# Kernel tuning notes

Hardware: AMD Instinct MI355X
Metric: run time of the kernel (lower is better)

The kernel has to match this reference:

```python
import jax, jax.numpy as jnp
import numpy as np

D_MODEL = 1024
N_HEADS = 16
D_K = D_MODEL // N_HEADS
D_FF = 4096
B, S = 2, 2048
LN_EPS = 1e-5
NEG_INF = -1e30  # finite stand-in for -inf; first (all-masked) row is overwritten by zeros anyway


def layer_norm(x, g, b):
    mu = jnp.mean(x, axis=-1, keepdims=True)
    var = jnp.mean(jnp.square(x - mu), axis=-1, keepdims=True)
    return (x - mu) * jax.lax.rsqrt(var + LN_EPS) * g + b


def setup_inputs() -> dict:
    key = jax.random.key(0)
    ks = jax.random.split(key, 16)
    sd = 0.02
    inp = {
        "query": jax.random.normal(ks[0], (B, S, D_MODEL), jnp.float32),
        "key": jax.random.normal(ks[1], (B, S, D_MODEL), jnp.float32),
        "values": jax.random.normal(ks[2], (B, S, D_MODEL), jnp.float32),
        "Wq": jax.random.normal(ks[3], (D_MODEL, D_MODEL), jnp.float32) * sd,
        "bq": jnp.zeros((D_MODEL,), jnp.float32),
        "Wk": jax.random.normal(ks[4], (D_MODEL, D_MODEL), jnp.float32) * sd,
        "bk": jnp.zeros((D_MODEL,), jnp.float32),
        "Wv": jax.random.normal(ks[5], (D_MODEL, D_MODEL), jnp.float32) * sd,
        "bv": jnp.zeros((D_MODEL,), jnp.float32),
        "Wo": jax.random.normal(ks[6], (D_MODEL, D_MODEL), jnp.float32) * sd,
        "bo": jnp.zeros((D_MODEL,), jnp.float32),
        "ln1_g": jnp.ones((D_MODEL,), jnp.float32),
        "ln1_b": jnp.zeros((D_MODEL,), jnp.float32),
        "W1": jax.random.normal(ks[7], (D_MODEL, D_FF), jnp.float32) * sd,
        "b1": jnp.zeros((D_FF,), jnp.float32),
        "W2": jax.random.normal(ks[8], (D_FF, D_MODEL), jnp.float32) * sd,
        "b2": jnp.zeros((D_MODEL,), jnp.float32),
        "ln2_g": jnp.ones((D_MODEL,), jnp.float32),
        "ln2_b": jnp.zeros((D_MODEL,), jnp.float32),
        "mask": 0,
    }
    return inp


def reference(query, key, values, Wq, bq, Wk, bk, Wv, bv, Wo, bo,
              ln1_g, ln1_b, W1, b1, W2, b2, ln2_g, ln2_b, mask):
    b, s, d = query.shape
    # projections -> [B, H, S, d_k]
    q = (query @ Wq + bq).reshape(b, s, N_HEADS, D_K).transpose(0, 2, 1, 3)
    k = (key @ Wk + bk).reshape(b, s, N_HEADS, D_K).transpose(0, 2, 1, 3)
    v = (values @ Wv + bv).reshape(b, s, N_HEADS, D_K).transpose(0, 2, 1, 3)
    # scores [B, H, S, S]
    scores = jnp.einsum("bhqd,bhkd->bhqk", q, k) / jnp.sqrt(jnp.float32(D_K))
    # torch: triu(ones, k=mask)==0 -> allowed iff j < i + mask
    i = jnp.arange(s)[:, None]
    j = jnp.arange(s)[None, :]
    allowed = j < (i + mask)
    scores = jnp.where(allowed, scores, NEG_INF)
    attn = jax.nn.softmax(scores, axis=-1)
    if mask == 0:
        # zero-pad trick: first query row (fully masked) is replaced by zeros
        attn = attn.at[:, :, 0, :].set(0.0)
    ctx = jnp.einsum("bhqk,bhkd->bhqd", attn, v)
    ctx = ctx.transpose(0, 2, 1, 3).reshape(b, s, d)
    attn_out = ctx @ Wo + bo
    x = layer_norm(query + attn_out, ln1_g, ln1_b)
    ffn = jax.nn.relu(x @ W1 + b1) @ W2 + b2
    out = layer_norm(x + ffn, ln2_g, ln2_b)
    return out
```

## Files before the change

### kernel.cpp

```cpp
#include <hip/hip_runtime.h>


typedef __attribute__((ext_vector_type(8))) __bf16 bf16x8;
typedef __attribute__((ext_vector_type(4))) float f32x4;
typedef __attribute__((ext_vector_type(8))) short s16x8;

struct alignas(8)  S4 { short x, y, z, w; };
struct alignas(16) F4 { float x, y, z, w; };

static __device__ __forceinline__ short f2bf(float f) {
  unsigned u = __float_as_uint(f);
  u += 0x7fff + ((u >> 16) & 1);
  return (short)(u >> 16);
}

static __device__ __forceinline__ short f2bf_fast(float f) {
  union { __bf16 h; short s; } u;
  u.h = (__bf16)f;
  return u.s;
}

#if __has_builtin(__builtin_amdgcn_exp2f)
#define EXP2F(x) __builtin_amdgcn_exp2f(x)
#else
#define EXP2F(x) exp2f(x)
#endif
#define SM_SCALE 0.18033688011112042f

static __device__ __forceinline__ void store_out(float* p, float v) { *p = v; }
static __device__ __forceinline__ void store_out(short* p, float v) { *p = f2bf(v); }

#define GLL16(g, l)                                                         \
  __builtin_amdgcn_global_load_lds(                                         \
      (__attribute__((address_space(1))) void*)(g),                         \
      (__attribute__((address_space(3))) void*)(l), 16, 0, 0)

__global__ __launch_bounds__(256) void cvt_bf16_kernel(
    const float* __restrict__ i0, const float* __restrict__ i1,
    const float* __restrict__ i2, short* __restrict__ o0,
    short* __restrict__ o1, short* __restrict__ o2) {
  int z = blockIdx.y;
  const float* in = z == 0 ? i0 : (z == 1 ? i1 : i2);
  short* out = z == 0 ? o0 : (z == 1 ? o1 : o2);
  int i = (blockIdx.x * 256 + threadIdx.x) * 4;
  F4 v = *(const F4*)(in + i);
  S4 o = { f2bf(v.x), f2bf(v.y), f2bf(v.z), f2bf(v.w) };
  *(S4*)(out + i) = o;
}

__global__ __launch_bounds__(256) void transpose_cvt_kernel(
    const float* __restrict__ Wq, const float* __restrict__ Wk,
    const float* __restrict__ Wv, const float* __restrict__ Wo,
    const float* __restrict__ W1, const float* __restrict__ W2,
    short* __restrict__ Wqt, short* __restrict__ Wkt,
    short* __restrict__ Wvt, short* __restrict__ Wot,
    short* __restrict__ W1t, short* __restrict__ W2t) {
  __shared__ float tile[64][65];
  int bid = blockIdx.x;
  const float* W; short* Wt; int K, N, kx, ny;
  if (bid < 1024) {
    int w = bid >> 8, t = bid & 255;
    W = w == 0 ? Wq : (w == 1 ? Wk : (w == 2 ? Wv : Wo));
    Wt = w == 0 ? Wqt : (w == 1 ? Wkt : (w == 2 ? Wvt : Wot));
    K = 1024; N = 1024; kx = t & 15; ny = t >> 4;
  } else if (bid < 2048) {
    int t = bid - 1024;
    W = W1; Wt = W1t; K = 1024; N = 4096; kx = t & 15; ny = t >> 4;
  } else {
    int t = bid - 2048;
    W = W2; Wt = W2t; K = 4096; N = 1024; kx = t & 63; ny = t >> 6;
  }
  int k0 = kx * 64, n0 = ny * 64;
  int tid = threadIdx.x;
  int rr = tid >> 4, cc = (tid & 15) * 4;
#pragma unroll
  for (int p = 0; p < 4; ++p) {
    int row = p * 16 + rr;
    F4 v = *(const F4*)&W[(long)(k0 + row) * N + n0 + cc];
    tile[row][cc] = v.x; tile[row][cc + 1] = v.y;
    tile[row][cc + 2] = v.z; tile[row][cc + 3] = v.w;
  }
  __syncthreads();
#pragma unroll
  for (int p = 0; p < 4; ++p) {
    int rn = p * 16 + rr;
    S4 o = { f2bf(tile[cc + 0][rn]), f2bf(tile[cc + 1][rn]),
             f2bf(tile[cc + 2][rn]), f2bf(tile[cc + 3][rn]) };
    *(S4*)&Wt[(long)(n0 + rn) * K + k0 + cc] = o;
  }
}

template <int NF, int OUT_MODE, bool RELU, typename OT>
__device__ __forceinline__ void gemm256_core(
    const short* __restrict__ A, const short* __restrict__ Bt,
    const float* __restrict__ bias, OT* __restrict__ out,
    int N, int K, int kBeg, int kEnd, int m0, int n0) {
  constexpr int BN = NF * 64;
  constexpr int LB = BN / 64;
  __shared__ __align__(16) short sA[2][256 * 64];
  __shared__ __align__(16) short sB[2][BN * 64];
  int tid = threadIdx.x;
  int lane = tid & 63, wave = tid >> 6;
  int col = lane & 15, quad = lane >> 4;
  int wm = (wave >> 2) * 128;
  int wn = (wave & 3) * (NF * 16);

  f32x4 acc[8][NF] = {};

  const int NT = (kEnd - kBeg) >> 6;
  const int t0 = kBeg >> 6;

  auto stageA = [&](int buf, int kt) {
#pragma unroll
    for (int j = 0; j < 4; ++j) {
      int idx = j * 512 + tid;
      int row = idx >> 3, cp = idx & 7;
      int c = cp ^ (row & 7);
      GLL16(A + (long)(m0 + row) * K + kt * 64 + c * 8,
            &sA[buf][(j * 512 + (wave << 6)) * 8]);
    }
  };
  auto stageB = [&](int buf, int kt) {
#pragma unroll
    for (int j = 0; j < LB; ++j) {
      int idx = j * 512 + tid;
      int row = idx >> 3, cp = idx & 7;
      int c = cp ^ (row & 7);
      GLL16(Bt + (long)(n0 + row) * K + kt * 64 + c * 8,
            &sB[buf][(j * 512 + (wave << 6)) * 8]);
    }
  };

  stageA(0, t0);     stageB(0, t0);
  stageA(1, t0 + 1); stageB(1, t0 + 1);
  if constexpr (NF == 4) asm volatile("s_waitcnt vmcnt(8)" ::: "memory");
  else                   asm volatile("s_waitcnt vmcnt(6)" ::: "memory");
  __builtin_amdgcn_sched_barrier(0);
  __builtin_amdgcn_s_barrier();

  for (int t = 0; t < NT; ++t) {
    int cur = t & 1;
    bool pf = (t + 2 < NT);
    bf16x8 bf[NF][2], af[2][2];

#pragma unroll
    for (int n = 0; n < NF; ++n) {
      int rb = wn + n * 16 + col;
#pragma unroll
      for (int kk = 0; kk < 2; ++kk) {
        int ca = kk * 4 + quad;
        bf[n][kk] = *(const bf16x8*)&sB[cur][rb * 64 + ((ca ^ (rb & 7)) << 3)];
      }
    }
#pragma unroll
    for (int i = 0; i < 2; ++i) {
      int ra = wm + i * 16 + col;
#pragma unroll
      for (int kk = 0; kk < 2; ++kk) {
        int ca = kk * 4 + quad;
        af[i][kk] = *(const bf16x8*)&sA[cur][ra * 64 + ((ca ^ (ra & 7)) << 3)];
      }
    }
    asm volatile("s_waitcnt lgkmcnt(0)" ::: "memory");
    __builtin_amdgcn_sched_barrier(0);
    __builtin_amdgcn_s_setprio(1);
#pragma unroll
    for (int i = 0; i < 2; ++i)
#pragma unroll
      for (int n = 0; n < NF; ++n)
#pragma unroll
        for (int kk = 0; kk < 2; ++kk)
          acc[i][n] = __builtin_amdgcn_mfma_f32_16x16x32_bf16(
              af[i][kk], bf[n][kk], acc[i][n], 0, 0, 0);
    __builtin_amdgcn_s_setprio(0);
    __builtin_amdgcn_s_barrier();
    __builtin_amdgcn_sched_barrier(0);

    if (pf) stageB(cur, t0 + t + 2);
#pragma unroll
    for (int i = 0; i < 2; ++i) {
      int ra = wm + (2 + i) * 16 + col;
#pragma unroll
      for (int kk = 0; kk < 2; ++kk) {
        int ca = kk * 4 + quad;
        af[i][kk] = *(const bf16x8*)&sA[cur][ra * 64 + ((ca ^ (ra & 7)) << 3)];
      }
    }
    __builtin_amdgcn_s_setprio(1);
#pragma unroll
    for (int i = 0; i < 2; ++i)
#pragma unroll
      for (int n = 0; n < NF; ++n)
#pragma unroll
        for (int kk = 0; kk < 2; ++kk)
          acc[2 + i][n] = __builtin_amdgcn_mfma_f32_16x16x32_bf16(
              af[i][kk], bf[n][kk], acc[2 + i][n], 0, 0, 0);
    __builtin_amdgcn_s_setprio(0);
    __builtin_amdgcn_s_barrier();

#pragma unroll
    for (int i = 0; i < 2; ++i) {
      int ra = wm + (4 + i) * 16 + col;
#pragma unroll
      for (int kk = 0; kk < 2; ++kk) {
        int ca = kk * 4 + quad;
        af[i][kk] = *(const bf16x8*)&sA[cur][ra * 64 + ((ca ^ (ra & 7)) << 3)];
      }
    }
    __builtin_amdgcn_s_setprio(1);
#pragma unroll
    for (int i = 0; i < 2; ++i)
#pragma unroll
      for (int n = 0; n < NF; ++n)
#pragma unroll
        for (int kk = 0; kk < 2; ++kk)
          acc[4 + i][n] = __builtin_amdgcn_mfma_f32_16x16x32_bf16(
              af[i][kk], bf[n][kk], acc[4 + i][n], 0, 0, 0);
    __builtin_amdgcn_s_setprio(0);
    __builtin_amdgcn_s_barrier();

#pragma unroll
    for (int i = 0; i < 2; ++i) {
      int ra = wm + (6 + i) * 16 + col;
#pragma unroll
      for (int kk = 0; kk < 2; ++kk) {
        int ca = kk * 4 + quad;
        af[i][kk] = *(const bf16x8*)&sA[cur][ra * 64 + ((ca ^ (ra & 7)) << 3)];
      }
    }
    asm volatile("s_waitcnt lgkmcnt(0)" ::: "memory");
    __builtin_amdgcn_sched_barrier(0);
    __builtin_amdgcn_s_barrier();
    __builtin_amdgcn_sched_barrier(0);
    if (pf) stageA(cur, t0 + t + 2);
    __builtin_amdgcn_s_setprio(1);
#pragma unroll
    for (int i = 0; i < 2; ++i)
#pragma unroll
      for (int n = 0; n < NF; ++n)
#pragma unroll
        for (int kk = 0; kk < 2; ++kk)
          acc[6 + i][n] = __builtin_amdgcn_mfma_f32_16x16x32_bf16(
              af[i][kk], bf[n][kk], acc[6 + i][n], 0, 0, 0);
    __builtin_amdgcn_s_setprio(0);
    if (pf) {
      if constexpr (NF == 4) asm volatile("s_waitcnt vmcnt(8)" ::: "memory");
      else                   asm volatile("s_waitcnt vmcnt(6)" ::: "memory");
    } else {
      asm volatile("s_waitcnt vmcnt(0)" ::: "memory");
    }
    __builtin_amdgcn_sched_barrier(0);
    __builtin_amdgcn_s_barrier();
  }

#pragma unroll
  for (int m = 0; m < 8; ++m) {
#pragma unroll
    for (int n = 0; n < NF; ++n) {
      int Cc = n0 + wn + n * 16 + col;
      float bv = bias ? bias[Cc] : 0.f;
#pragma unroll
      for (int r = 0; r < 4; ++r) {
        int R = m0 + wm + m * 16 + quad * 4 + r;
        float v = acc[m][n][r] + bv;
        if (RELU) v = v > 0.f ? v : 0.f;
        if (OUT_MODE == 0) {
          store_out(&out[(long)R * N + Cc], v);
        } else {
          int bb = R >> 11, s = R & 2047, h = Cc >> 6, d = Cc & 63;
          store_out(&out[((long)((bb * 16 + h) * 2048 + s) << 6) + d], v);
        }
      }
    }
  }
}

__device__ __forceinline__ void gsp128_core(
    const short* __restrict__ A, const short* __restrict__ Bt,
    const float* __restrict__ bias, float* __restrict__ out,
    int N, int K, int kBeg, int kEnd, int m0, int n0) {
  __shared__ __align__(16) short sA[2][256 * 64];
  __shared__ __align__(16) short sB[2][128 * 64];
  int tid = threadIdx.x;
  int lane = tid & 63, wave = tid >> 6;
  int col = lane & 15, quad = lane >> 4;
  int wm = (wave >> 1) * 64;
  int wn = (wave & 1) * 64;

  f32x4 acc[4][4] = {};
  const int NT = (kEnd - kBeg) >> 6;
  const int t0 = kBeg >> 6;

  auto stageA = [&](int buf, int kt) {
#pragma unroll
    for (int j = 0; j < 4; ++j) {
      int idx = j * 512 + tid;
      int row = idx >> 3, cp = idx & 7;
      int c = cp ^ (row & 7);
      GLL16(A + (long)(m0 + row) * K + kt * 64 + c * 8,
            &sA[buf][(j * 512 + (wave << 6)) * 8]);
    }
  };
  auto stageB = [&](int buf, int kt) {
#pragma unroll
    for (int j = 0; j < 2; ++j) {
      int idx = j * 512 + tid;
      int row = idx >> 3, cp = idx & 7;
      int c = cp ^ (row & 7);
      GLL16(Bt + (long)(n0 + row) * K + kt * 64 + c * 8,
            &sB[buf][(j * 512 + (wave << 6)) * 8]);
    }
  };

  stageA(0, t0);     stageB(0, t0);
  stageA(1, t0 + 1); stageB(1, t0 + 1);
  asm volatile("s_waitcnt vmcnt(6)" ::: "memory");
  __builtin_amdgcn_s_barrier();

  for (int t = 0; t < NT; ++t) {
    int cur = t & 1;
    bool pf = (t + 2 < NT);
    bf16x8 bf[4][2], af[4][2];

#pragma unroll
    for (int n = 0; n < 4; ++n) {
      int rb = wn + n * 16 + col;
#pragma unroll
      for (int kk = 0; kk < 2; ++kk) {
        int ca = kk * 4 + quad;
        bf[n][kk] = *(const bf16x8*)&sB[cur][rb * 64 + ((ca ^ (rb & 7)) << 3)];
      }
    }
#pragma unroll
    for (int m = 0; m < 4; ++m) {
      int ra = wm + m * 16 + col;
#pragma unroll
      for (int kk = 0; kk < 2; ++kk) {
        int ca = kk * 4 + quad;
        af[m][kk] = *(const bf16x8*)&sA[cur][ra * 64 + ((ca ^ (ra & 7)) << 3)];
      }
    }
    asm volatile("s_waitcnt lgkmcnt(0)" ::: "memory");
    __builtin_amdgcn_s_barrier();
    __builtin_amdgcn_sched_barrier(0);
    if (pf) { stageA(cur, t0 + t + 2); stageB(cur, t0 + t + 2); }
    __builtin_amdgcn_s_setprio(1);
#pragma unroll
    for (int m = 0; m < 4; ++m)
#pragma unroll
      for (int n = 0; n < 4; ++n)
#pragma unroll
        for (int kk = 0; kk < 2; ++kk)
          acc[m][n] = __builtin_amdgcn_mfma_f32_16x16x32_bf16(
              af[m][kk], bf[n][kk], acc[m][n], 0, 0, 0);
    __builtin_amdgcn_s_setprio(0);
    if (pf) asm volatile("s_waitcnt vmcnt(6)" ::: "memory");
    else    asm volatile("s_waitcnt vmcnt(0)" ::: "memory");
    __builtin_amdgcn_s_barrier();
  }

#pragma unroll
  for (int m = 0; m < 4; ++m) {
#pragma unroll
    for (int n = 0; n < 4; ++n) {
      int Cc = n0 + wn + n * 16 + col;
      float bv = bias ? bias[Cc] : 0.f;
#pragma unroll
      for (int r = 0; r < 4; ++r) {
        int R = m0 + wm + m * 16 + quad * 4 + r;
        out[(long)R * N + Cc] = acc[m][n][r] + bv;
      }
    }
  }
}

__global__ __launch_bounds__(512) void g256_ffn1(
    const short* __restrict__ A, const short* __restrict__ Bt,
    const float* __restrict__ bias, short* __restrict__ out) {
  gemm256_core<4, 0, true, short>(A, Bt, bias, out, 4096, 1024, 0, 1024,
                                  blockIdx.x * 256, blockIdx.y * 256);
}

__global__ __launch_bounds__(512) void g256_qkv(
    const short* __restrict__ Aq, const short* __restrict__ Ak,
    const short* __restrict__ Av, const short* __restrict__ Btq,
    const short* __restrict__ Btk, const short* __restrict__ Btv,
    const float* __restrict__ bq, const float* __restrict__ bk,
    const float* __restrict__ bv, short* __restrict__ Qp,
    short* __restrict__ Kp, short* __restrict__ Vp) {
  int z = blockIdx.z;
  const short* A = z == 0 ? Aq : (z == 1 ? Ak : Av);
  const short* Bt = z == 0 ? Btq : (z == 1 ? Btk : Btv);
  const float* bias = z == 0 ? bq : (z == 1 ? bk : bv);
  short* out = z == 0 ? Qp : (z == 1 ? Kp : Vp);
  gemm256_core<4, 1, false, short>(A, Bt, bias, out, 1024, 1024, 0, 1024,
                                   blockIdx.x * 256, blockIdx.y * 256);
}

__global__ __launch_bounds__(512) void gsp_wo(
    const short* __restrict__ A, const short* __restrict__ Bt,
    const float* __restrict__ bias, float* __restrict__ p0,
    float* __restrict__ p1) {
  int z = blockIdx.z;
  float* out = z == 0 ? p0 : p1;
  const float* b = z == 0 ? bias : nullptr;
  gsp128_core(A, Bt, b, out, 1024, 1024, z * 512, z * 512 + 512,
              blockIdx.x * 256, blockIdx.y * 128);
}

__global__ __launch_bounds__(512) void gsp_ffn2(
    const short* __restrict__ A, const short* __restrict__ Bt,
    const float* __restrict__ bias, float* __restrict__ p0,
    float* __restrict__ p1) {
  int z = blockIdx.z;
  float* out = z == 0 ? p0 : p1;
  const float* b = z == 0 ? bias : nullptr;
  gsp128_core(A, Bt, b, out, 1024, 4096, z * 2048, z * 2048 + 2048,
              blockIdx.x * 256, blockIdx.y * 128);
}

__global__ __launch_bounds__(256) void attn_kernel(
    const short* __restrict__ Q, const short* __restrict__ K,
    const short* __restrict__ V, const int* __restrict__ maskp,
    short* __restrict__ ctx) {
  __shared__ __align__(16) short sK[2][64 * 64];
  __shared__ __align__(16) int   sVt[2][64 * 32];
  __shared__ __align__(16) short sP[4 * 32 * 64];
  __shared__ float sLred[64];
  int tid = threadIdx.x, wave = tid >> 6;
  int lane = tid & 63;
  int col = lane & 15, quad = lane >> 4;
  int wlow = wave >> 1, g = wave & 1;
  int bh = blockIdx.x, pair = blockIdx.y;
  int maskv = maskp[0];
  const long base = (long)bh * (2048 * 64);
  int b = bh >> 4, h = bh & 15;

  int kp = tid & 31, dg = tid >> 5, d0v = dg * 8;

  for (int pass = 0; pass < 2; ++pass) {
    int qt = pass ? (31 - pair) : pair;
    int iq0 = qt * 64 + wlow * 32;

    long jmax = (long)qt * 64 + 63 + maskv - 1;
    int tot = (jmax < 0) ? 0 : (int)(jmax >> 6) + 1;
    if (tot > 32) tot = 32;

    bf16x8 aQ[2][2];
#pragma unroll
    for (int mt = 0; mt < 2; ++mt)
#pragma unroll
      for (int kk = 0; kk < 2; ++kk)
        aQ[mt][kk] = *(const bf16x8*)&Q[base +
            (long)(iq0 + mt * 16 + col) * 64 + kk * 32 + quad * 8];

    f32x4 o[2][4] = {};
    float lsum[2][4] = {};

    if (tot > 0) {
#pragma unroll
      for (int j = 0; j < 2; ++j) {
        int idx = j * 256 + tid;
        int row = idx >> 3, cp = idx & 7;
        int c = cp ^ (row & 7);
        GLL16(K + base + (long)row * 64 + c * 8,
              &sK[0][(j * 256 + (wave << 6)) * 8]);
      }
      {
        s16x8 u0 = *(const s16x8*)&V[base + (long)(2 * kp) * 64 + d0v];
        s16x8 u1 = *(const s16x8*)&V[base + (long)(2 * kp + 1) * 64 + d0v];
#pragma unroll
        for (int j = 0; j < 8; ++j) {
          int d = d0v + j;
          int w = ((int)(unsigned short)u1[j] << 16) | (unsigned short)u0[j];
          sVt[0][d * 32 + ((((kp >> 2) ^ (d & 7)) << 2) | (kp & 3))] = w;
        }
      }
    }
    __syncthreads();

    for (int kt = 0; kt < tot; ++kt) {
      int cur = kt & 1, nxt = cur ^ 1;
      bool pf = (kt + 1 < tot);

      s16x8 u0, u1;
      if (pf) {
#pragma unroll
        for (int j = 0; j < 2; ++j) {
          int idx = j * 256 + tid;
          int row = idx >> 3, cp = idx & 7;
          int c = cp ^ (row & 7);
          GLL16(K + base + (long)((kt + 1) * 64 + row) * 64 + c * 8,
                &sK[nxt][(j * 256 + (wave << 6)) * 8]);
        }
        u0 = *(const s16x8*)&V[base + (long)((kt + 1) * 64 + 2 * kp) * 64 + d0v];
        u1 = *(const s16x8*)&V[base + (long)((kt + 1) * 64 + 2 * kp + 1) * 64 + d0v];
      }

      f32x4 sc[2][2] = {};
      __builtin_amdgcn_s_setprio(1);
#pragma unroll
      for (int kk = 0; kk < 2; ++kk) {
        int ca = kk * 4 + quad;
#pragma unroll
        for (int nt = 0; nt < 2; ++nt) {
          int rk = (2 * g + nt) * 16 + col;
          bf16x8 bK = *(const bf16x8*)&sK[cur][rk * 64 + ((ca ^ (rk & 7)) << 3)];
#pragma unroll
          for (int mt = 0; mt < 2; ++mt)
            sc[mt][nt] = __builtin_amdgcn_mfma_f32_16x16x32_bf16(
                aQ[mt][kk], bK, sc[mt][nt], 0, 0, 0);
        }
      }
      __builtin_amdgcn_s_setprio(0);

      bool interior = (kt * 64 + g * 32 + 31) < (iq0 + maskv);
      if (interior) {
#pragma unroll
        for (int mt = 0; mt < 2; ++mt)
#pragma unroll
          for (int r = 0; r < 4; ++r) {
            int qr = mt * 16 + quad * 4 + r;
#pragma unroll
            for (int nt = 0; nt < 2; ++nt) {
              float p = EXP2F(sc[mt][nt][r] * SM_SCALE);
              lsum[mt][r] += p;
              int k8 = 4 * g + nt * 2 + (col >> 3);
              sP[wave * 2048 + qr * 64 + (((k8 ^ (qr & 7)) << 3) | (col & 7))] =
                  f2bf_fast(p);
            }
          }
      } else {
#pragma unroll
        for (int mt = 0; mt < 2; ++mt)
#pragma unroll
          for (int r = 0; r < 4; ++r) {
            int i = iq0 + mt * 16 + quad * 4 + r;
            int qr = mt * 16 + quad * 4 + r;
#pragma unroll
            for (int nt = 0; nt < 2; ++nt) {
              int j = kt * 64 + (2 * g + nt) * 16 + col;
              float p = (j < i + maskv) ? EXP2F(sc[mt][nt][r] * SM_SCALE) : 0.f;
              lsum[mt][r] += p;
              int k8 = 4 * g + nt * 2 + (col >> 3);
              sP[wave * 2048 + qr * 64 + (((k8 ^ (qr & 7)) << 3) | (col & 7))] =
                  f2bf_fast(p);
            }
          }
      }

      {
        int ca = 4 * g + quad;
        bf16x8 bV[4];
#pragma unroll
        for (int dt = 0; dt < 4; ++dt) {
          int d = dt * 16 + col;
          bV[dt] = *(const bf16x8*)((const short*)sVt[cur] + d * 64 +
                                    ((ca ^ (d & 7)) << 3));
        }
        __builtin_amdgcn_s_setprio(1);
#pragma unroll
        for (int mt = 0; mt < 2; ++mt) {
          int rp = mt * 16 + col;
          bf16x8 aP = *(const bf16x8*)&sP[wave * 2048 + rp * 64 +
                                          ((ca ^ (rp & 7)) << 3)];
#pragma unroll
          for (int dt = 0; dt < 4; ++dt)
            o[mt][dt] = __builtin_amdgcn_mfma_f32_16x16x32_bf16(
                aP, bV[dt], o[mt][dt], 0, 0, 0);
        }
        __builtin_amdgcn_s_setprio(0);
      }

      if (pf) {
#pragma unroll
        for (int j = 0; j < 8; ++j) {
          int d = d0v + j;
          int w = ((int)(unsigned short)u1[j] << 16) | (unsigned short)u0[j];
          sVt[nxt][d * 32 + ((((kp >> 2) ^ (d & 7)) << 2) | (kp & 3))] = w;
        }
      }
      __syncthreads();
    }

#pragma unroll
    for (int mt = 0; mt < 2; ++mt)
#pragma unroll
      for (int r = 0; r < 4; ++r)
#pragma unroll
        for (int off = 1; off < 16; off <<= 1)
          lsum[mt][r] += __shfl_xor(lsum[mt][r], off);

    f32x4* odv = (f32x4*)sP;
    int slot = wlow * 64 + lane;
    if (g == 1) {
#pragma unroll
      for (int mt = 0; mt < 2; ++mt)
#pragma unroll
        for (int dt = 0; dt < 4; ++dt)
          odv[(mt * 4 + dt) * 128 + slot] = o[mt][dt];
      if (col == 0) {
#pragma unroll
        for (int mt = 0; mt < 2; ++mt)
#pragma unroll
          for (int r = 0; r < 4; ++r)
            sLred[wlow * 32 + mt * 16 + quad * 4 + r] = lsum[mt][r];
      }
    }
    __syncthreads();
    if (g == 0) {
#pragma unroll
      for (int mt = 0; mt < 2; ++mt)
#pragma unroll
        for (int dt = 0; dt < 4; ++dt)
          o[mt][dt] += odv[(mt * 4 + dt) * 128 + slot];
#pragma unroll
      for (int mt = 0; mt < 2; ++mt)
#pragma unroll
        for (int r = 0; r < 4; ++r) {
          float ls = lsum[mt][r] + sLred[wlow * 32 + mt * 16 + quad * 4 + r];
          int i = iq0 + mt * 16 + quad * 4 + r;
          float inv = (ls > 0.f) ? 1.f / ls : 0.f;
          if (maskv == 0 && i == 0) inv = 0.f;
#pragma unroll
          for (int dt = 0; dt < 4; ++dt)
            ctx[(long)(b * 2048 + i) * 1024 + h * 64 + dt * 16 + col] =
                f2bf(o[mt][dt][r] * inv);
        }
    }
    __syncthreads();
  }
}

__global__ __launch_bounds__(256) void ln_comb_kernel(
    const float* __restrict__ p0, const float* __restrict__ p1,
    const float* __restrict__ res, const float* __restrict__ g,
    const float* __restrict__ b, float* __restrict__ outf,
    short* __restrict__ outb) {
  int r = blockIdx.x, tid = threadIdx.x;
  int lane = tid & 63, wave = tid >> 6;
  long off0 = (long)r * 1024;
  F4 a = ((const F4*)(p0 + off0))[tid];
  F4 c = ((const F4*)(p1 + off0))[tid];
  F4 d = ((const F4*)(res + off0))[tid];
  F4 v = { a.x + c.x + d.x, a.y + c.y + d.y, a.z + c.z + d.z, a.w + c.w + d.w };
  float s = v.x + v.y + v.z + v.w;
  float sq = v.x * v.x + v.y * v.y + v.z * v.z + v.w * v.w;
#pragma unroll
  for (int off = 1; off < 64; off <<= 1) {
    s += __shfl_xor(s, off);
    sq += __shfl_xor(sq, off);
  }
  __shared__ float rs[4], rq[4];
  if (lane == 0) { rs[wave] = s; rq[wave] = sq; }
  __syncthreads();
  s = rs[0] + rs[1] + rs[2] + rs[3];
  sq = rq[0] + rq[1] + rq[2] + rq[3];
  float mu = s * (1.0f / 1024.0f);
  float var = sq * (1.0f / 1024.0f) - mu * mu;
  float rstd = rsqrtf(var + 1e-5f);
  F4 gv = ((const F4*)g)[tid], bv = ((const F4*)b)[tid];
  F4 o;
  o.x = (v.x - mu) * rstd * gv.x + bv.x;
  o.y = (v.y - mu) * rstd * gv.y + bv.y;
  o.z = (v.z - mu) * rstd * gv.z + bv.z;
  o.w = (v.w - mu) * rstd * gv.w + bv.w;
  ((F4*)(outf + off0))[tid] = o;
  if (outb) {
    S4 ob = { f2bf(o.x), f2bf(o.y), f2bf(o.z), f2bf(o.w) };
    ((S4*)(outb + off0))[tid] = ob;
  }
}

extern "C" void kernel_launch(void* const* d_in, const int* in_sizes, int n_in,
                              void* d_out, int out_size, void* d_ws, size_t ws_size,
                              hipStream_t stream) {
  const float* query  = (const float*)d_in[0];
  const float* keyi   = (const float*)d_in[1];
  const float* values = (const float*)d_in[2];
  const float* Wq = (const float*)d_in[3];
  const float* bq = (const float*)d_in[4];
  const float* Wk = (const float*)d_in[5];
  const float* bk = (const float*)d_in[6];
  const float* Wv = (const float*)d_in[7];
  const float* bv = (const float*)d_in[8];
  const float* Wo = (const float*)d_in[9];
  const float* bo = (const float*)d_in[10];
  const float* ln1_g = (const float*)d_in[11];
  const float* ln1_b = (const float*)d_in[12];
  const float* W1 = (const float*)d_in[13];
  const float* b1 = (const float*)d_in[14];
  const float* W2 = (const float*)d_in[15];
  const float* b2 = (const float*)d_in[16];
  const float* ln2_g = (const float*)d_in[17];
  const float* ln2_b = (const float*)d_in[18];
  const int*   maskp = (const int*)d_in[19];
  float* out = (float*)d_out;

  char* ws = (char*)d_ws;
  const size_t MB = 1u << 20;
  short* q_bf = (short*)(ws + 0);
  short* k_bf = (short*)(ws + 8 * MB);
  short* v_bf = (short*)(ws + 16 * MB);
  short* ctx  = (short*)(ws + 24 * MB);
  short* Qp   = (short*)(ws + 32 * MB);
  short* Kp   = (short*)(ws + 40 * MB);
  short* Vp   = (short*)(ws + 48 * MB);
  short* Wqt  = (short*)(ws + 56 * MB);
  short* Wkt  = (short*)(ws + 58 * MB);
  short* Wvt  = (short*)(ws + 60 * MB);
  short* Wot  = (short*)(ws + 62 * MB);
  short* W1t  = (short*)(ws + 64 * MB);
  short* W2t  = (short*)(ws + 72 * MB);
  short* hbuf = (short*)(ws + 80 * MB);
  float* pWo0 = (float*)(ws + 0);
  float* pWo1 = (float*)(ws + 32 * MB);
  float* x_f32 = (float*)(ws + 16 * MB);
  short* x_bf  = (short*)(ws + 48 * MB);
  float* pF0 = (float*)(ws + 0);
  float* pF1 = (float*)(ws + 32 * MB);

  cvt_bf16_kernel<<<dim3(4096, 3), 256, 0, stream>>>(query, keyi, values,
                                                     q_bf, k_bf, v_bf);
  transpose_cvt_kernel<<<3072, 256, 0, stream>>>(Wq, Wk, Wv, Wo, W1, W2,
                                                 Wqt, Wkt, Wvt, Wot, W1t, W2t);
  g256_qkv<<<dim3(16, 4, 3), 512, 0, stream>>>(q_bf, k_bf, v_bf,
                                               Wqt, Wkt, Wvt,
                                               bq, bk, bv, Qp, Kp, Vp);
  attn_kernel<<<dim3(32, 16), 256, 0, stream>>>(Qp, Kp, Vp, maskp, ctx);
  gsp_wo<<<dim3(16, 8, 2), 512, 0, stream>>>(ctx, Wot, bo, pWo0, pWo1);
  ln_comb_kernel<<<4096, 256, 0, stream>>>(pWo0, pWo1, query, ln1_g, ln1_b,
                                           x_f32, x_bf);
  g256_ffn1<<<dim3(16, 16), 512, 0, stream>>>(x_bf, W1t, b1, hbuf);
  gsp_ffn2<<<dim3(16, 8, 2), 512, 0, stream>>>(hbuf, W2t, b2, pF0, pF1);
  ln_comb_kernel<<<4096, 256, 0, stream>>>(pF0, pF1, x_f32, ln2_g, ln2_b,
                                           out, nullptr);

  (void)in_sizes; (void)n_in; (void)out_size; (void)ws_size;
}
```

Before: 371.1 us.

## Collapse 256x256 GEMM main loop into single load-all/compute-all phase per k-tile

Replaces the four-phase interleaved k-loop (A fragments loaded in pairs, with MFMA groups, barriers and staggered A/B prefetches between them) with a simpler schedule. Each k-tile now loads all A and B fragments from LDS, issues one barrier, prefetches both A and B for tile t+2, then runs all 64 MFMAs. This cuts barriers per iteration from four to two and removes the sched_barrier fences. In exchange it needs more registers for the 16 A fragments, and it gives up overlap of LDS reads with MFMA work, which may reduce occupancy or lengthen the issue latency.

```diff
diff --git a/kernel.cpp b/kernel.cpp
--- a/kernel.cpp
+++ b/kernel.cpp
@@ -90,23 +90,20 @@
   }
 }
 
-template <int NF, int OUT_MODE, bool RELU, typename OT>
-__device__ __forceinline__ void gemm256_core(
+template <int OUT_MODE, bool RELU, typename OT>
+__device__ __forceinline__ void gemm256c_core(
     const short* __restrict__ A, const short* __restrict__ Bt,
     const float* __restrict__ bias, OT* __restrict__ out,
     int N, int K, int kBeg, int kEnd, int m0, int n0) {
-  constexpr int BN = NF * 64;
-  constexpr int LB = BN / 64;
   __shared__ __align__(16) short sA[2][256 * 64];
-  __shared__ __align__(16) short sB[2][BN * 64];
+  __shared__ __align__(16) short sB[2][256 * 64];
   int tid = threadIdx.x;
   int lane = tid & 63, wave = tid >> 6;
   int col = lane & 15, quad = lane >> 4;
   int wm = (wave >> 2) * 128;
-  int wn = (wave & 3) * (NF * 16);
-
-  f32x4 acc[8][NF] = {};
-
+  int wn = (wave & 3) * 64;
+
+  f32x4 acc[8][4] = {};
   const int NT = (kEnd - kBeg) >> 6;
   const int t0 = kBeg >> 6;
 
@@ -122,7 +119,7 @@
   };
   auto stageB = [&](int buf, int kt) {
 #pragma unroll
-    for (int j = 0; j < LB; ++j) {
+    for (int j = 0; j < 4; ++j) {
       int idx = j * 512 + tid;
       int row = idx >> 3, cp = idx & 7;
       int c = cp ^ (row & 7);
@@ -133,18 +130,16 @@
 
   stageA(0, t0);     stageB(0, t0);
   stageA(1, t0 + 1); stageB(1, t0 + 1);
-  if constexpr (NF == 4) asm volatile("s_waitcnt vmcnt(8)" ::: "memory");
-  else                   asm volatile("s_waitcnt vmcnt(6)" ::: "memory");
-  __builtin_amdgcn_sched_barrier(0);
+  asm volatile("s_waitcnt vmcnt(8)" ::: "memory");
   __builtin_amdgcn_s_barrier();
 
   for (int t = 0; t < NT; ++t) {
     int cur = t & 1;
     bool pf = (t + 2 < NT);
-    bf16x8 bf[NF][2], af[2][2];
-
-#pragma unroll
-    for (int n = 0; n < NF; ++n) {
+    bf16x8 bf[4][2], af[8][2];
+
+#pragma unroll
+    for (int n = 0; n < 4; ++n) {
       int rb = wn + n * 16 + col;
 #pragma unroll
       for (int kk = 0; kk < 2; ++kk) {
@@ -153,110 +148,37 @@
       }
     }
 #pragma unroll
-    for (int i = 0; i < 2; ++i) {
-      int ra = wm + i * 16 + col;
+    for (int m = 0; m < 8; ++m) {
+      int ra = wm + m * 16 + col;
 #pragma unroll
       for (int kk = 0; kk < 2; ++kk) {
         int ca = kk * 4 + quad;
-        af[i][kk] = *(const bf16x8*)&sA[cur][ra * 64 + ((ca ^ (ra & 7)) << 3)];
+        af[m][kk] = *(const bf16x8*)&sA[cur][ra * 64 + ((ca ^ (ra & 7)) << 3)];
       }
     }
     asm volatile("s_waitcnt lgkmcnt(0)" ::: "memory");
-    __builtin_amdgcn_sched_barrier(0);
-    __builtin_amdgcn_s_setprio(1);
-#pragma unroll
-    for (int i = 0; i < 2; ++i)
-#pragma unroll
-      for (int n = 0; n < NF; ++n)
-#pragma unroll
-        for (int kk = 0; kk < 2; ++kk)
-          acc[i][n] = __builtin_amdgcn_mfma_f32_16x16x32_bf16(
-              af[i][kk], bf[n][kk], acc[i][n], 0, 0, 0);
-    __builtin_amdgcn_s_setprio(0);
     __builtin_amdgcn_s_barrier();
     __builtin_amdgcn_sched_barrier(0);
-
-    if (pf) stageB(cur, t0 + t + 2);
-#pragma unroll
-    for (int i = 0; i < 2; ++i) {
-      int ra = wm + (2 + i) * 16 + col;
-#pragma unroll
-      for (int kk = 0; kk < 2; ++kk) {
-        int ca = kk * 4 + quad;
-        af[i][kk] = *(const bf16x8*)&sA[cur][ra * 64 + ((ca ^ (ra & 7)) << 3)];
-      }
-    }
+    if (pf) { stageA(cur, t0 + t + 2); stageB(cur, t0 + t + 2); }
     __builtin_amdgcn_s_setprio(1);
 #pragma unroll
-    for (int i = 0; i < 2; ++i)
-#pragma unroll
-      for (int n = 0; n < NF; ++n)
+    for (int m = 0; m < 8; ++m)
+#pragma unroll
+      for (int n = 0; n < 4; ++n)
 #pragma unroll
         for (int kk = 0; kk < 2; ++kk)
-          acc[2 + i][n] = __builtin_amdgcn_mfma_f32_16x16x32_bf16(
-              af[i][kk], bf[n][kk], acc[2 + i][n], 0, 0, 0);
+          acc[m][n] = __builtin_amdgcn_mfma_f32_16x16x32_bf16(
+              af[m][kk], bf[n][kk], acc[m][n], 0, 0, 0);
     __builtin_amdgcn_s_setprio(0);
+    if (pf) asm volatile("s_waitcnt vmcnt(8)" ::: "memory");
+    else    asm volatile("s_waitcnt vmcnt(0)" ::: "memory");
     __builtin_amdgcn_s_barrier();
-
-#pragma unroll
-    for (int i = 0; i < 2; ++i) {
-      int ra = wm + (4 + i) * 16 + col;
-#pragma unroll
-      for (int kk = 0; kk < 2; ++kk) {
-        int ca = kk * 4 + quad;
-        af[i][kk] = *(const bf16x8*)&sA[cur][ra * 64 + ((ca ^ (ra & 7)) << 3)];
-      }
-    }
-    __builtin_amdgcn_s_setprio(1);
-#pragma unroll
-    for (int i = 0; i < 2; ++i)
-#pragma unroll
-      for (int n = 0; n < NF; ++n)
-#pragma unroll
-        for (int kk = 0; kk < 2; ++kk)
-          acc[4 + i][n] = __builtin_amdgcn_mfma_f32_16x16x32_bf16(
-              af[i][kk], bf[n][kk], acc[4 + i][n], 0, 0, 0);
-    __builtin_amdgcn_s_setprio(0);
-    __builtin_amdgcn_s_barrier();
-
-#pragma unroll
-    for (int i = 0; i < 2; ++i) {
-      int ra = wm + (6 + i) * 16 + col;
-#pragma unroll
-      for (int kk = 0; kk < 2; ++kk) {
-        int ca = kk * 4 + quad;
-        af[i][kk] = *(const bf16x8*)&sA[cur][ra * 64 + ((ca ^ (ra & 7)) << 3)];
-      }
-    }
-    asm volatile("s_waitcnt lgkmcnt(0)" ::: "memory");
-    __builtin_amdgcn_sched_barrier(0);
-    __builtin_amdgcn_s_barrier();
-    __builtin_amdgcn_sched_barrier(0);
-    if (pf) stageA(cur, t0 + t + 2);
-    __builtin_amdgcn_s_setprio(1);
-#pragma unroll
-    for (int i = 0; i < 2; ++i)
-#pragma unroll
-      for (int n = 0; n < NF; ++n)
-#pragma unroll
-        for (int kk = 0; kk < 2; ++kk)
-          acc[6 + i][n] = __builtin_amdgcn_mfma_f32_16x16x32_bf16(
-              af[i][kk], bf[n][kk], acc[6 + i][n], 0, 0, 0);
-    __builtin_amdgcn_s_setprio(0);
-    if (pf) {
-      if constexpr (NF == 4) asm volatile("s_waitcnt vmcnt(8)" ::: "memory");
-      else                   asm volatile("s_waitcnt vmcnt(6)" ::: "memory");
-    } else {
-      asm volatile("s_waitcnt vmcnt(0)" ::: "memory");
-    }
-    __builtin_amdgcn_sched_barrier(0);
-    __builtin_amdgcn_s_barrier();
   }
 
 #pragma unroll
   for (int m = 0; m < 8; ++m) {
 #pragma unroll
-    for (int n = 0; n < NF; ++n) {
+    for (int n = 0; n < 4; ++n) {
       int Cc = n0 + wn + n * 16 + col;
       float bv = bias ? bias[Cc] : 0.f;
 #pragma unroll
@@ -374,14 +296,14 @@
   }
 }
 
-__global__ __launch_bounds__(512) void g256_ffn1(
+__global__ __launch_bounds__(512) void g256c_ffn1(
     const short* __restrict__ A, const short* __restrict__ Bt,
     const float* __restrict__ bias, short* __restrict__ out) {
-  gemm256_core<4, 0, true, short>(A, Bt, bias, out, 4096, 1024, 0, 1024,
-                                  blockIdx.x * 256, blockIdx.y * 256);
-}
-
-__global__ __launch_bounds__(512) void g256_qkv(
+  gemm256c_core<0, true, short>(A, Bt, bias, out, 4096, 1024, 0, 1024,
+                                blockIdx.x * 256, blockIdx.y * 256);
+}
+
+__global__ __launch_bounds__(512) void g256c_qkv(
     const short* __restrict__ Aq, const short* __restrict__ Ak,
     const short* __restrict__ Av, const short* __restrict__ Btq,
     const short* __restrict__ Btk, const short* __restrict__ Btv,
@@ -393,8 +315,8 @@
   const short* Bt = z == 0 ? Btq : (z == 1 ? Btk : Btv);
   const float* bias = z == 0 ? bq : (z == 1 ? bk : bv);
   short* out = z == 0 ? Qp : (z == 1 ? Kp : Vp);
-  gemm256_core<4, 1, false, short>(A, Bt, bias, out, 1024, 1024, 0, 1024,
-                                   blockIdx.x * 256, blockIdx.y * 256);
+  gemm256c_core<1, false, short>(A, Bt, bias, out, 1024, 1024, 0, 1024,
+                                 blockIdx.x * 256, blockIdx.y * 256);
 }
 
 __global__ __launch_bounds__(512) void gsp_wo(
@@ -724,14 +646,14 @@
                                                      q_bf, k_bf, v_bf);
   transpose_cvt_kernel<<<3072, 256, 0, stream>>>(Wq, Wk, Wv, Wo, W1, W2,
                                                  Wqt, Wkt, Wvt, Wot, W1t, W2t);
-  g256_qkv<<<dim3(16, 4, 3), 512, 0, stream>>>(q_bf, k_bf, v_bf,
-                                               Wqt, Wkt, Wvt,
-                                               bq, bk, bv, Qp, Kp, Vp);
+  g256c_qkv<<<dim3(16, 4, 3), 512, 0, stream>>>(q_bf, k_bf, v_bf,
+                                                Wqt, Wkt, Wvt,
+                                                bq, bk, bv, Qp, Kp, Vp);
   attn_kernel<<<dim3(32, 16), 256, 0, stream>>>(Qp, Kp, Vp, maskp, ctx);
   gsp_wo<<<dim3(16, 8, 2), 512, 0, stream>>>(ctx, Wot, bo, pWo0, pWo1);
   ln_comb_kernel<<<4096, 256, 0, stream>>>(pWo0, pWo1, query, ln1_g, ln1_b,
                                            x_f32, x_bf);
-  g256_ffn1<<<dim3(16, 16), 512, 0, stream>>>(x_bf, W1t, b1, hbuf);
+  g256c_ffn1<<<dim3(16, 16), 512, 0, stream>>>(x_bf, W1t, b1, hbuf);
   gsp_ffn2<<<dim3(16, 8, 2), 512, 0, stream>>>(hbuf, W2t, b2, pF0, pF1);
   ln_comb_kernel<<<4096, 256, 0, stream>>>(pF0, pF1, x_f32, ln2_g, ln2_b,
                                            out, nullptr);
```

Measured after the change: 370.4 us. About the same (-0.2%).
